# Kernel tuning notes

Measured on AMD Instinct MI355X. Metric: run time of the kernel, lower is better.

Reference implementation:

```python
import jax, jax.numpy as jnp
import numpy as np

CS = 128            # config.chunk_size
K = 8               # config.k + 1
EPS = 1e-6          # config.eps
L = K * CS          # extended_len = 1024


def setup_inputs() -> dict:
    key = jax.random.key(0)
    k1, k2 = jax.random.split(key)
    B, T, E = 2, 8192, 256
    x = jax.random.normal(k1, (B, T, E), dtype=jnp.float32)
    # xavier_normal_ on [CS, L]: std = sqrt(2 / (fan_in + fan_out))
    std = np.sqrt(2.0 / (CS + L)).astype(np.float32)
    down_proj = jax.random.normal(k2, (CS, L), dtype=jnp.float32) * std
    return {"x": x, "down_proj": down_proj}


def reference(x, down_proj):
    B, T, E = x.shape
    N = T // CS  # T chosen divisible by CS, so the pad branch is a no-op
    chunks = x.reshape(B, N, CS, E)

    # --- per-chunk retrieval scores (vectorized over the causal chunk loop) ---
    cn = chunks / (jnp.linalg.norm(chunks, axis=-1, keepdims=True) + EPS)
    # row-wise cosine sims between every pair of chunks: [B,N,N,CS,CS]
    sims = jnp.einsum('bice,bjde->bijcd', cn, cn)
    scores = sims.max(axis=-1).sum(axis=-1)              # [B,N,N]
    i_idx = jnp.arange(N)
    causal = i_idx[None, :] < i_idx[:, None]             # j < i allowed
    NEG = jnp.asarray(-1e9, x.dtype)
    scores = jnp.where(causal[None], scores, NEG)

    # --- topk selection, weights (num_sel_i = min(i, K-1)) ---
    vals, idx = jax.lax.top_k(scores, K - 1)             # descending, [B,N,K-1]
    num_sel = jnp.minimum(i_idx, K - 1)                  # [N]
    vmin_slot = jnp.clip(num_sel - 1, 0, K - 2)          # last valid slot = min of topk vals
    v_min = jnp.take_along_axis(vals, jnp.broadcast_to(vmin_slot[None, :, None], (B, N, 1)), axis=-1)
    slot = jnp.arange(K - 1)
    valid = slot[None, :] < num_sel[:, None]             # [N,K-1]
    w = jnp.where(valid[None], vals / (v_min + EPS), 0.0)  # [B,N,K-1]

    # --- weighted gather of selected chunks ---
    b_idx = jnp.arange(B)[:, None, None]
    sel = chunks[b_idx, idx]                             # [B,N,K-1,CS,E]
    weighted = sel * w[..., None, None]

    # --- left-pad to L: zeros occupy leftmost slots, then topk-ordered chunks, then cur ---
    shift = jnp.maximum(0, (K - 1) - i_idx)              # [N]
    src = jnp.clip(slot[None, :] - shift[:, None], 0, K - 2)   # [N,K-1]
    n_idx = jnp.arange(N)[None, :, None]
    arranged = weighted[b_idx, n_idx, src[None]]         # [B,N,K-1,CS,E]
    keep = slot[None, :] >= shift[:, None]
    arranged = jnp.where(keep[None, :, :, None, None], arranged, 0.0)

    ext = jnp.concatenate([arranged.reshape(B, N, (K - 1) * CS, E), chunks], axis=2)  # [B,N,L,E]
    # down_proj @ ext + x_chunks, then contract back to [B,T,E]
    out = jnp.einsum('cl,bnle->bnce', down_proj, ext) + chunks
    return out.reshape(B, N * CS, E)
```

## Files before the change

kernel.cpp:

```cpp
#include <hip/hip_runtime.h>
#include <hip/hip_bf16.h>

#define CS     128
#define EDIM   256
#define NBATCH 2
#define TLEN   8192
#define NCHUNK 64
#define LEXT   1024
#define KSEL   7

typedef __attribute__((ext_vector_type(8))) short   short8;
typedef __attribute__((ext_vector_type(4))) float   floatx4;

__device__ inline short bf16_of(float f) {
    __hip_bfloat16 h = __float2bfloat16(f);
    return *(short*)&h;
}
__device__ inline float f_of_bf16(short s) {
    __hip_bfloat16 h = *(__hip_bfloat16*)&s;
    return __bfloat162float(h);
}

__device__ inline void gl_lds16(const void* g, void* l) {
    __builtin_amdgcn_global_load_lds(
        (const __attribute__((address_space(1))) unsigned int*)g,
        (__attribute__((address_space(3))) unsigned int*)l, 16, 0, 0);
}

__global__ __launch_bounds__(256) void prep_kernel(const float* __restrict__ x,
                                                   const float* __restrict__ dp,
                                                   short* __restrict__ cn_hi,
                                                   short* __restrict__ cn_lo,
                                                   short* __restrict__ xt_hi,
                                                   short* __restrict__ dp_hi) {
    const int bx = blockIdx.x;
    if (bx >= 256) {
        int t = (bx - 256) * 256 + threadIdx.x;
#pragma unroll
        for (int u = 0; u < 16; ++u) {
            int idx = (t * 16 + u) * 4;
            float4 v = *(const float4*)(dp + idx);
            *(short4*)(dp_hi + idx) =
                make_short4(bf16_of(v.x), bf16_of(v.y), bf16_of(v.z), bf16_of(v.w));
        }
        return;
    }

    __shared__ float tile[64 * 257];
    const int b = bx >> 7, t0 = (bx & 127) * 64;
    const int tid = threadIdx.x;
    const int r = tid >> 2, q = tid & 3;

    const float* src = x + ((size_t)(b * TLEN + t0 + r)) * EDIM + q * 64;
    float* trow = &tile[r * 257 + q * 64];
    float s = 0.f;
#pragma unroll
    for (int u = 0; u < 16; ++u) {
        float4 v = *(const float4*)(src + u * 4);
        s += v.x * v.x + v.y * v.y + v.z * v.z + v.w * v.w;
        trow[u * 4 + 0] = v.x; trow[u * 4 + 1] = v.y;
        trow[u * 4 + 2] = v.z; trow[u * 4 + 3] = v.w;
    }
    s += __shfl_xor(s, 1);
    s += __shfl_xor(s, 2);
    const float rn = 1.0f / (sqrtf(s) + 1e-6f);

    short* ch = cn_hi + ((size_t)(b * TLEN + t0 + r)) * EDIM + q * 64;
    short* cl = cn_lo + ((size_t)(b * TLEN + t0 + r)) * EDIM + q * 64;
#pragma unroll
    for (int u = 0; u < 16; ++u) {
        short hs[4], ls[4];
#pragma unroll
        for (int k2 = 0; k2 < 4; ++k2) {
            float c = trow[u * 4 + k2] * rn;
            hs[k2] = bf16_of(c);
            ls[k2] = bf16_of(c - f_of_bf16(hs[k2]));
        }
        *(short4*)(ch + u * 4) = make_short4(hs[0], hs[1], hs[2], hs[3]);
        *(short4*)(cl + u * 4) = make_short4(ls[0], ls[1], ls[2], ls[3]);
    }
    __syncthreads();

    const int g16 = tid >> 4, tq = tid & 15;
#pragma unroll
    for (int it = 0; it < 16; ++it) {
        int e = g16 + it * 16;
        short hs2[4];
#pragma unroll
        for (int g = 0; g < 4; ++g)
            hs2[g] = bf16_of(tile[(tq * 4 + g) * 257 + e]);
        *(short4*)(xt_hi + ((size_t)(b * EDIM + e)) * TLEN + t0 + tq * 4)
            = make_short4(hs2[0], hs2[1], hs2[2], hs2[3]);
    }
}

__global__ __launch_bounds__(256) void scores_mfma(const short* __restrict__ cn_hi,
                                                   const short* __restrict__ cn_lo,
                                                   float* __restrict__ scores) {
    __shared__ short tiles[4][4096];
    double* red2  = (double*)&tiles[0][0];
    float*  redbuf = (float*)&tiles[0][8];

    const int p = blockIdx.x, b = blockIdx.y;
    int i = (int)((1.0f + sqrtf(1.0f + 8.0f * (float)p)) * 0.5f);
    while (i * (i - 1) / 2 > p) --i;
    while (i * (i + 1) / 2 <= p) ++i;
    const int j = p - i * (i - 1) / 2;

    const int tid  = threadIdx.x;
    const int w    = tid >> 6, lane = tid & 63;
    const int wr   = w >> 1, wc = w & 1;
    const int quad = lane >> 4, l15 = lane & 15;

    const short* sarr  = (w & 1) ? cn_lo : cn_hi;
    const size_t sbase = ((size_t)b * TLEN + ((w >> 1) ? j : i) * CS) * EDIM;
    const int rr  = lane >> 2;
    const int c16 = (lane & 3) * 8;
    const int csw = c16 ^ (((rr >> 1) & 3) * 8);
    const int q8  = (quad ^ ((l15 >> 1) & 3)) * 8;

    floatx4 acc[4][4];
#pragma unroll
    for (int rt = 0; rt < 4; ++rt)
#pragma unroll
        for (int ct = 0; ct < 4; ++ct) acc[rt][ct] = (floatx4){0.f, 0.f, 0.f, 0.f};

    for (int ks = 0; ks < 8; ++ks) {
        const short* gsrc = sarr + sbase + ks * 32 + csw;
        short* ldst = &tiles[w][0];
#pragma unroll
        for (int t = 0; t < 8; ++t)
            gl_lds16(gsrc + (size_t)(16 * t + rr) * EDIM, ldst + t * 512);
        __syncthreads();

        short8 bh[4], bl[4];
#pragma unroll
        for (int ct = 0; ct < 4; ++ct) {
            int r = wc * 64 + ct * 16 + l15;
            bh[ct] = *(const short8*)&tiles[2][r * 32 + q8];
            bl[ct] = *(const short8*)&tiles[3][r * 32 + q8];
        }
#pragma unroll
        for (int rt = 0; rt < 4; ++rt) {
            int r = wr * 64 + rt * 16 + l15;
            short8 ah = *(const short8*)&tiles[0][r * 32 + q8];
            short8 al = *(const short8*)&tiles[1][r * 32 + q8];
#pragma unroll
            for (int ct = 0; ct < 4; ++ct) {
                acc[rt][ct] = __builtin_amdgcn_mfma_f32_16x16x32_bf16(ah, bh[ct], acc[rt][ct], 0, 0, 0);
                acc[rt][ct] = __builtin_amdgcn_mfma_f32_16x16x32_bf16(ah, bl[ct], acc[rt][ct], 0, 0, 0);
                acc[rt][ct] = __builtin_amdgcn_mfma_f32_16x16x32_bf16(al, bh[ct], acc[rt][ct], 0, 0, 0);
            }
        }
        __syncthreads();
    }

#pragma unroll
    for (int rt = 0; rt < 4; ++rt) {
        float m[4];
#pragma unroll
        for (int reg = 0; reg < 4; ++reg) {
            float mm = acc[rt][0][reg];
#pragma unroll
            for (int ct = 1; ct < 4; ++ct) mm = fmaxf(mm, acc[rt][ct][reg]);
            m[reg] = mm;
        }
#pragma unroll
        for (int off = 1; off < 16; off <<= 1)
#pragma unroll
            for (int reg = 0; reg < 4; ++reg) m[reg] = fmaxf(m[reg], __shfl_xor(m[reg], off));
        if (l15 == 0) {
#pragma unroll
            for (int reg = 0; reg < 4; ++reg)
                redbuf[wc * 128 + wr * 64 + rt * 16 + quad * 4 + reg] = m[reg];
        }
    }
    __syncthreads();

    double part = 0.0;
    if (tid < 128) part = (double)fmaxf(redbuf[tid], redbuf[128 + tid]);
#pragma unroll
    for (int off = 1; off < 64; off <<= 1) part += __shfl_xor(part, off);
    if (lane == 0 && w < 2) red2[w] = part;
    __syncthreads();
    if (tid == 0) scores[(b * NCHUNK + i) * NCHUNK + j] = (float)(red2[0] + red2[1]);
}

__global__ __launch_bounds__(256) void out_mfma(const float* __restrict__ x,
                                                const short* __restrict__ dph,
                                                const short* __restrict__ xth,
                                                const float* __restrict__ scores,
                                                float* __restrict__ out) {
    __shared__ short As[2][128 * 32];
    __shared__ short Bs[2][64 * 32];
    __shared__ int   slist[8], sslot[8], snum;
    __shared__ float swei[8];

    const int eq = blockIdx.x, n = blockIdx.y, b = blockIdx.z;
    const int e0 = eq * 64;
    const int tid  = threadIdx.x;
    const int w    = tid >> 6, lane = tid & 63;
    const int wr   = w >> 1, wc = w & 1;
    const int quad = lane >> 4, l15 = lane & 15;
    const int rr   = lane >> 2;
    const int c16  = (lane & 3) * 8;
    const int csw  = c16 ^ (((rr >> 1) & 3) * 8);
    const int q8   = (quad ^ ((l15 >> 1) & 3)) * 8;

    if (w == 0) {
        const float* srow = scores + (b * NCHUNK + n) * NCHUNK;
        const int nsel = n < KSEL ? n : KSEL;
        float v = (lane < n) ? srow[lane] : -3.0e38f;
        float vals[KSEL];
        int   idxs[KSEL];
        for (int s2 = 0; s2 < nsel; ++s2) {
            float bv = v; int bi = lane;
#pragma unroll
            for (int off = 1; off < 64; off <<= 1) {
                float ov = __shfl_xor(bv, off);
                int   oi = __shfl_xor(bi, off);
                if (ov > bv || (ov == bv && oi < bi)) { bv = ov; bi = oi; }
            }
            vals[s2] = bv; idxs[s2] = bi;
            if (lane == bi) v = -3.0e38f;
        }
        if (lane == 0) {
            float vmin = (nsel > 0) ? vals[nsel - 1] : 0.0f;
            float inv  = 1.0f / (vmin + 1e-6f);
            int shift  = KSEL - nsel;
            int c = 0;
            for (int s2 = 0; s2 < 8; ++s2) {
                int jj; float ww;
                if (s2 < KSEL) {
                    int tt = s2 - shift;
                    if (tt >= 0) { jj = idxs[tt]; ww = vals[tt] * inv; }
                    else         { jj = -1;       ww = 0.0f; }
                } else { jj = n; ww = 1.0f; }
                if (jj >= 0) { slist[c] = jj; sslot[c] = s2; swei[c] = ww; ++c; }
            }
            snum = c;
        }
    }
    __syncthreads();
    const int NS = snum * 4;

    auto stage = [&](int st, int bf) {
        int sv = st >> 2, kk = st & 3;
        if (w < 2) {
            const short* gsrc = dph + (size_t)(sslot[sv] * 128 + kk * 32) + csw;
#pragma unroll
            for (int t = 0; t < 4; ++t)
                gl_lds16(gsrc + (size_t)(w * 64 + t * 16 + rr) * LEXT,
                         &As[bf][(w * 64 + t * 16) * 32]);
        } else {
            const short* gsrc = xth + ((size_t)(b * EDIM + e0)) * TLEN
                                + (size_t)(slist[sv] * CS + kk * 32) + csw;
#pragma unroll
            for (int t = 0; t < 2; ++t)
                gl_lds16(gsrc + (size_t)((w - 2) * 32 + t * 16 + rr) * TLEN,
                         &Bs[bf][((w - 2) * 32 + t * 16) * 32]);
        }
    };

    floatx4 accT[4][2], accP[4][2];
#pragma unroll
    for (int rt = 0; rt < 4; ++rt)
#pragma unroll
        for (int ct = 0; ct < 2; ++ct) accT[rt][ct] = (floatx4){0.f, 0.f, 0.f, 0.f};

    stage(0, 0);
    __syncthreads();

    int buf = 0;
    for (int st = 0; st < NS; ++st) {
        if (st + 1 < NS) stage(st + 1, buf ^ 1);

        if ((st & 3) == 0) {
#pragma unroll
            for (int rt = 0; rt < 4; ++rt)
#pragma unroll
                for (int ct = 0; ct < 2; ++ct) accP[rt][ct] = (floatx4){0.f, 0.f, 0.f, 0.f};
        }

        short8 bh[2];
#pragma unroll
        for (int ct = 0; ct < 2; ++ct) {
            int e = wc * 32 + ct * 16 + l15;
            bh[ct] = *(const short8*)&Bs[buf][e * 32 + q8];
        }
#pragma unroll
        for (int rt = 0; rt < 4; ++rt) {
            int r = wr * 64 + rt * 16 + l15;
            short8 ah = *(const short8*)&As[buf][r * 32 + q8];
#pragma unroll
            for (int ct = 0; ct < 2; ++ct)
                accP[rt][ct] = __builtin_amdgcn_mfma_f32_16x16x32_bf16(ah, bh[ct], accP[rt][ct], 0, 0, 0);
        }

        if ((st & 3) == 3) {
            float wcur = swei[st >> 2];
#pragma unroll
            for (int rt = 0; rt < 4; ++rt)
#pragma unroll
                for (int ct = 0; ct < 2; ++ct)
#pragma unroll
                    for (int reg = 0; reg < 4; ++reg)
                        accT[rt][ct][reg] += wcur * accP[rt][ct][reg];
        }
        __syncthreads();
        buf ^= 1;
    }

#pragma unroll
    for (int rt = 0; rt < 4; ++rt)
#pragma unroll
        for (int ct = 0; ct < 2; ++ct) {
#pragma unroll
            for (int reg = 0; reg < 4; ++reg) {
                int row = wr * 64 + rt * 16 + quad * 4 + reg;
                int col = wc * 32 + ct * 16 + l15;
                size_t o = ((size_t)(b * TLEN + n * CS + row)) * EDIM + e0 + col;
                out[o] = accT[rt][ct][reg] + x[o];
            }
        }
}

extern "C" void kernel_launch(void* const* d_in, const int* in_sizes, int n_in,
                              void* d_out, int out_size, void* d_ws, size_t ws_size,
                              hipStream_t stream) {
    const float* x  = (const float*)d_in[0];
    const float* dp = (const float*)d_in[1];
    float* out = (float*)d_out;

    char* ws = (char*)d_ws;
    short* cn_hi  = (short*)(ws);
    short* cn_lo  = (short*)(ws + (8u << 20));
    short* xt_hi  = (short*)(ws + (16u << 20));
    short* dp_hi  = (short*)(ws + (24u << 20));
    float* scores = (float*)(ws + (25u << 20));

    prep_kernel <<<dim3(264), 256, 0, stream>>>(x, dp, cn_hi, cn_lo, xt_hi, dp_hi);
    scores_mfma <<<dim3(NCHUNK * (NCHUNK - 1) / 2, NBATCH), 256, 0, stream>>>(cn_hi, cn_lo, scores);
    out_mfma    <<<dim3(4, NCHUNK, NBATCH), 256, 0, stream>>>(x, dp_hi, xt_hi, scores, out);
}
```

Before: 214.0 us.

## Fuse three kernels into one persistent cooperative kernel with grid syncs

Merges the prep, scores and output phases into a single cooperative persistent kernel that loops over work units with grid-stride loops and separates the phases with grid-wide barriers. The goal is to drop the launch gaps and tail effects between the three kernels. The prep phase is also restructured: row normalisation now uses one wave per row with shuffle reductions, and the transpose uses smaller 64x64 tiles. The cost is grid-sync overhead, occupancy capped by the 32KB shared buffer, and fewer blocks than the original scores launch. It falls back to the old three-launch path if the cooperative launch fails.

```diff
diff --git a/kernel.cpp b/kernel.cpp
--- a/kernel.cpp
+++ b/kernel.cpp
@@ -1,5 +1,8 @@
 #include <hip/hip_runtime.h>
 #include <hip/hip_bf16.h>
+#include <hip/hip_cooperative_groups.h>
+
+namespace cg = cooperative_groups;
 
 #define CS     128
 #define EDIM   256
@@ -25,6 +28,300 @@
     __builtin_amdgcn_global_load_lds(
         (const __attribute__((address_space(1))) unsigned int*)g,
         (__attribute__((address_space(3))) unsigned int*)l, 16, 0, 0);
+}
+
+__global__ __launch_bounds__(256) void mega_kernel(const float* __restrict__ x,
+                                                   const float* __restrict__ dp,
+                                                   short* __restrict__ cn_hi,
+                                                   short* __restrict__ cn_lo,
+                                                   short* __restrict__ xt_hi,
+                                                   short* __restrict__ dp_hi,
+                                                   float* __restrict__ scores,
+                                                   float* __restrict__ out) {
+    __shared__ __align__(16) char smem[32768];
+    cg::grid_group gg = cg::this_grid();
+
+    const int tid  = threadIdx.x;
+    const int bid  = blockIdx.x;
+    const int gdim = gridDim.x;
+    const int w    = tid >> 6, lane = tid & 63;
+    const int quad = lane >> 4, l15 = lane & 15;
+    const int rr   = lane >> 2, c16 = (lane & 3) * 8;
+    const int csw  = c16 ^ (((rr >> 1) & 3) * 8);
+    const int q8   = (quad ^ ((l15 >> 1) & 3)) * 8;
+
+    for (int u = bid; u < 2056; u += gdim) {
+        if (u < 1024) {
+#pragma unroll
+            for (int pass = 0; pass < 4; ++pass) {
+                int row = u * 16 + w * 4 + pass;
+                const float4 v = ((const float4*)(x + (size_t)row * EDIM))[lane];
+                float s = v.x * v.x + v.y * v.y + v.z * v.z + v.w * v.w;
+#pragma unroll
+                for (int off = 1; off < 64; off <<= 1) s += __shfl_xor(s, off);
+                float rn = 1.0f / (sqrtf(s) + 1e-6f);
+                float c[4] = {v.x * rn, v.y * rn, v.z * rn, v.w * rn};
+                short hs[4], ls[4];
+#pragma unroll
+                for (int q = 0; q < 4; ++q) {
+                    hs[q] = bf16_of(c[q]);
+                    ls[q] = bf16_of(c[q] - f_of_bf16(hs[q]));
+                }
+                size_t o = (size_t)row * EDIM + lane * 4;
+                *(short4*)(cn_hi + o) = make_short4(hs[0], hs[1], hs[2], hs[3]);
+                *(short4*)(cn_lo + o) = make_short4(ls[0], ls[1], ls[2], ls[3]);
+            }
+        } else if (u < 1032) {
+            int t = (u - 1024) * 256 + tid;
+#pragma unroll
+            for (int k = 0; k < 16; ++k) {
+                int idx = (t * 16 + k) * 4;
+                float4 v = *(const float4*)(dp + idx);
+                *(short4*)(dp_hi + idx) =
+                    make_short4(bf16_of(v.x), bf16_of(v.y), bf16_of(v.z), bf16_of(v.w));
+            }
+        } else {
+            float* tile = (float*)smem;
+            int ut = u - 1032;
+            int b2 = ut >> 9, et = (ut >> 7) & 3, tt2 = ut & 127;
+            int e0 = et * 64, t0 = tt2 * 64;
+            int r2 = tid >> 2, c4 = (tid & 3) * 16;
+            const float* src = x + ((size_t)(b2 * TLEN + t0 + r2)) * EDIM + e0 + c4;
+#pragma unroll
+            for (int k = 0; k < 4; ++k)
+                *(float4*)&tile[r2 * 68 + c4 + k * 4] = *(const float4*)(src + k * 4);
+            __syncthreads();
+            int e = tid >> 2, tq = tid & 3;
+            short hs2[16];
+#pragma unroll
+            for (int g = 0; g < 16; ++g) hs2[g] = bf16_of(tile[(tq * 16 + g) * 68 + e]);
+            short* xd = xt_hi + ((size_t)(b2 * EDIM + e0 + e)) * TLEN + t0 + tq * 16;
+#pragma unroll
+            for (int q4 = 0; q4 < 4; ++q4)
+                *(short4*)(xd + q4 * 4) =
+                    make_short4(hs2[q4*4], hs2[q4*4+1], hs2[q4*4+2], hs2[q4*4+3]);
+            __syncthreads();
+        }
+    }
+    gg.sync();
+
+    {
+        short (*tiles)[4096] = (short(*)[4096])smem;
+        double* red2  = (double*)smem;
+        float*  redbuf = (float*)(smem + 16);
+
+        for (int u = bid; u < 4032; u += gdim) {
+            const int b = u & 1, p = u >> 1;
+            int i = (int)((1.0f + sqrtf(1.0f + 8.0f * (float)p)) * 0.5f);
+            while (i * (i - 1) / 2 > p) --i;
+            while (i * (i + 1) / 2 <= p) ++i;
+            const int j = p - i * (i - 1) / 2;
+
+            const short* sarr  = (w & 1) ? cn_lo : cn_hi;
+            const size_t sbase = ((size_t)b * TLEN + ((w >> 1) ? j : i) * CS) * EDIM;
+            const int wr = w >> 1, wc = w & 1;
+
+            floatx4 acc[4][4];
+#pragma unroll
+            for (int rt = 0; rt < 4; ++rt)
+#pragma unroll
+                for (int ct = 0; ct < 4; ++ct) acc[rt][ct] = (floatx4){0.f, 0.f, 0.f, 0.f};
+
+            for (int ks = 0; ks < 8; ++ks) {
+                const short* gsrc = sarr + sbase + ks * 32 + csw;
+                short* ldst = &tiles[w][0];
+#pragma unroll
+                for (int t = 0; t < 8; ++t)
+                    gl_lds16(gsrc + (size_t)(16 * t + rr) * EDIM, ldst + t * 512);
+                __syncthreads();
+
+                short8 bh[4], bl[4];
+#pragma unroll
+                for (int ct = 0; ct < 4; ++ct) {
+                    int r = wc * 64 + ct * 16 + l15;
+                    bh[ct] = *(const short8*)&tiles[2][r * 32 + q8];
+                    bl[ct] = *(const short8*)&tiles[3][r * 32 + q8];
+                }
+#pragma unroll
+                for (int rt = 0; rt < 4; ++rt) {
+                    int r = wr * 64 + rt * 16 + l15;
+                    short8 ah = *(const short8*)&tiles[0][r * 32 + q8];
+                    short8 al = *(const short8*)&tiles[1][r * 32 + q8];
+#pragma unroll
+                    for (int ct = 0; ct < 4; ++ct) {
+                        acc[rt][ct] = __builtin_amdgcn_mfma_f32_16x16x32_bf16(ah, bh[ct], acc[rt][ct], 0, 0, 0);
+                        acc[rt][ct] = __builtin_amdgcn_mfma_f32_16x16x32_bf16(ah, bl[ct], acc[rt][ct], 0, 0, 0);
+                        acc[rt][ct] = __builtin_amdgcn_mfma_f32_16x16x32_bf16(al, bh[ct], acc[rt][ct], 0, 0, 0);
+                    }
+                }
+                __syncthreads();
+            }
+
+#pragma unroll
+            for (int rt = 0; rt < 4; ++rt) {
+                float m[4];
+#pragma unroll
+                for (int reg = 0; reg < 4; ++reg) {
+                    float mm = acc[rt][0][reg];
+#pragma unroll
+                    for (int ct = 1; ct < 4; ++ct) mm = fmaxf(mm, acc[rt][ct][reg]);
+                    m[reg] = mm;
+                }
+#pragma unroll
+                for (int off = 1; off < 16; off <<= 1)
+#pragma unroll
+                    for (int reg = 0; reg < 4; ++reg) m[reg] = fmaxf(m[reg], __shfl_xor(m[reg], off));
+                if (l15 == 0) {
+#pragma unroll
+                    for (int reg = 0; reg < 4; ++reg)
+                        redbuf[wc * 128 + wr * 64 + rt * 16 + quad * 4 + reg] = m[reg];
+                }
+            }
+            __syncthreads();
+
+            double part = 0.0;
+            if (tid < 128) part = (double)fmaxf(redbuf[tid], redbuf[128 + tid]);
+#pragma unroll
+            for (int off = 1; off < 64; off <<= 1) part += __shfl_xor(part, off);
+            if (lane == 0 && w < 2) red2[w] = part;
+            __syncthreads();
+            if (tid == 0) scores[(b * NCHUNK + i) * NCHUNK + j] = (float)(red2[0] + red2[1]);
+        }
+    }
+    gg.sync();
+
+    {
+        short* As    = (short*)smem;
+        short* Bs    = (short*)(smem + 16384);
+        int*   slist = (int*)(smem + 24576);
+        int*   sslot = (int*)(smem + 24608);
+        float* swei  = (float*)(smem + 24640);
+        int*   snum  = (int*)(smem + 24672);
+
+        for (int u = bid; u < 512; u += gdim) {
+            const int eq = u & 3, n = (u >> 2) & 63, b = u >> 8;
+            const int e0 = eq * 64;
+            const int wr = w >> 1, wc = w & 1;
+
+            if (w == 0) {
+                const float* srow = scores + (b * NCHUNK + n) * NCHUNK;
+                const int nsel = n < KSEL ? n : KSEL;
+                float v = (lane < n) ? srow[lane] : -3.0e38f;
+                float vals[KSEL];
+                int   idxs[KSEL];
+                for (int s2 = 0; s2 < nsel; ++s2) {
+                    float bv = v; int bi = lane;
+#pragma unroll
+                    for (int off = 1; off < 64; off <<= 1) {
+                        float ov = __shfl_xor(bv, off);
+                        int   oi = __shfl_xor(bi, off);
+                        if (ov > bv || (ov == bv && oi < bi)) { bv = ov; bi = oi; }
+                    }
+                    vals[s2] = bv; idxs[s2] = bi;
+                    if (lane == bi) v = -3.0e38f;
+                }
+                if (lane == 0) {
+                    float vmin = (nsel > 0) ? vals[nsel - 1] : 0.0f;
+                    float inv  = 1.0f / (vmin + 1e-6f);
+                    int shift  = KSEL - nsel;
+                    int c = 0;
+                    for (int s2 = 0; s2 < 8; ++s2) {
+                        int jj; float ww;
+                        if (s2 < KSEL) {
+                            int tt = s2 - shift;
+                            if (tt >= 0) { jj = idxs[tt]; ww = vals[tt] * inv; }
+                            else         { jj = -1;       ww = 0.0f; }
+                        } else { jj = n; ww = 1.0f; }
+                        if (jj >= 0) { slist[c] = jj; sslot[c] = s2; swei[c] = ww; ++c; }
+                    }
+                    *snum = c;
+                }
+            }
+            __syncthreads();
+            const int NS = (*snum) * 4;
+
+            auto stage = [&](int st, int bf) {
+                int sv = st >> 2, kk = st & 3;
+                if (w < 2) {
+                    const short* gsrc = dp_hi + (size_t)(sslot[sv] * 128 + kk * 32) + csw;
+#pragma unroll
+                    for (int t = 0; t < 4; ++t)
+                        gl_lds16(gsrc + (size_t)(w * 64 + t * 16 + rr) * LEXT,
+                                 As + bf * 4096 + (w * 64 + t * 16) * 32);
+                } else {
+                    const short* gsrc = xt_hi + ((size_t)(b * EDIM + e0)) * TLEN
+                                        + (size_t)(slist[sv] * CS + kk * 32) + csw;
+#pragma unroll
+                    for (int t = 0; t < 2; ++t)
+                        gl_lds16(gsrc + (size_t)((w - 2) * 32 + t * 16 + rr) * TLEN,
+                                 Bs + bf * 2048 + ((w - 2) * 32 + t * 16) * 32);
+                }
+            };
+
+            floatx4 accT[4][2], accP[4][2];
+#pragma unroll
+            for (int rt = 0; rt < 4; ++rt)
+#pragma unroll
+                for (int ct = 0; ct < 2; ++ct) accT[rt][ct] = (floatx4){0.f, 0.f, 0.f, 0.f};
+
+            stage(0, 0);
+            __syncthreads();
+
+            int buf = 0;
+            for (int st = 0; st < NS; ++st) {
+                if (st + 1 < NS) stage(st + 1, buf ^ 1);
+
+                if ((st & 3) == 0) {
+#pragma unroll
+                    for (int rt = 0; rt < 4; ++rt)
+#pragma unroll
+                        for (int ct = 0; ct < 2; ++ct) accP[rt][ct] = (floatx4){0.f, 0.f, 0.f, 0.f};
+                }
+
+                short8 bh[2];
+#pragma unroll
+                for (int ct = 0; ct < 2; ++ct) {
+                    int e = wc * 32 + ct * 16 + l15;
+                    bh[ct] = *(const short8*)&Bs[buf * 2048 + e * 32 + q8];
+                }
+#pragma unroll
+                for (int rt = 0; rt < 4; ++rt) {
+                    int r = wr * 64 + rt * 16 + l15;
+                    short8 ah = *(const short8*)&As[buf * 4096 + r * 32 + q8];
+#pragma unroll
+                    for (int ct = 0; ct < 2; ++ct)
+                        accP[rt][ct] = __builtin_amdgcn_mfma_f32_16x16x32_bf16(ah, bh[ct], accP[rt][ct], 0, 0, 0);
+                }
+
+                if ((st & 3) == 3) {
+                    float wcur = swei[st >> 2];
+#pragma unroll
+                    for (int rt = 0; rt < 4; ++rt)
+#pragma unroll
+                        for (int ct = 0; ct < 2; ++ct)
+#pragma unroll
+                            for (int reg = 0; reg < 4; ++reg)
+                                accT[rt][ct][reg] += wcur * accP[rt][ct][reg];
+                }
+                __syncthreads();
+                buf ^= 1;
+            }
+
+#pragma unroll
+            for (int rt = 0; rt < 4; ++rt)
+#pragma unroll
+                for (int ct = 0; ct < 2; ++ct) {
+#pragma unroll
+                    for (int reg = 0; reg < 4; ++reg) {
+                        int row = wr * 64 + rt * 16 + quad * 4 + reg;
+                        int col = wc * 32 + ct * 16 + l15;
+                        size_t o = ((size_t)(b * TLEN + n * CS + row)) * EDIM + e0 + col;
+                        out[o] = accT[rt][ct][reg] + x[o];
+                    }
+                }
+            __syncthreads();
+        }
+    }
 }
 
 __global__ __launch_bounds__(256) void prep_kernel(const float* __restrict__ x,
@@ -45,12 +342,10 @@
         }
         return;
     }
-
     __shared__ float tile[64 * 257];
     const int b = bx >> 7, t0 = (bx & 127) * 64;
     const int tid = threadIdx.x;
     const int r = tid >> 2, q = tid & 3;
-
     const float* src = x + ((size_t)(b * TLEN + t0 + r)) * EDIM + q * 64;
     float* trow = &tile[r * 257 + q * 64];
     float s = 0.f;
@@ -64,7 +359,6 @@
     s += __shfl_xor(s, 1);
     s += __shfl_xor(s, 2);
     const float rn = 1.0f / (sqrtf(s) + 1e-6f);
-
     short* ch = cn_hi + ((size_t)(b * TLEN + t0 + r)) * EDIM + q * 64;
     short* cl = cn_lo + ((size_t)(b * TLEN + t0 + r)) * EDIM + q * 64;
 #pragma unroll
@@ -80,7 +374,6 @@
         *(short4*)(cl + u * 4) = make_short4(ls[0], ls[1], ls[2], ls[3]);
     }
     __syncthreads();
-
     const int g16 = tid >> 4, tq = tid & 15;
 #pragma unroll
     for (int it = 0; it < 16; ++it) {
@@ -111,7 +404,6 @@
     const int w    = tid >> 6, lane = tid & 63;
     const int wr   = w >> 1, wc = w & 1;
     const int quad = lane >> 4, l15 = lane & 15;
-
     const short* sarr  = (w & 1) ? cn_lo : cn_hi;
     const size_t sbase = ((size_t)b * TLEN + ((w >> 1) ? j : i) * CS) * EDIM;
     const int rr  = lane >> 2;
@@ -132,7 +424,6 @@
         for (int t = 0; t < 8; ++t)
             gl_lds16(gsrc + (size_t)(16 * t + rr) * EDIM, ldst + t * 512);
         __syncthreads();
-
         short8 bh[4], bl[4];
 #pragma unroll
         for (int ct = 0; ct < 4; ++ct) {
@@ -154,7 +445,6 @@
         }
         __syncthreads();
     }
-
 #pragma unroll
     for (int rt = 0; rt < 4; ++rt) {
         float m[4];
@@ -176,7 +466,6 @@
         }
     }
     __syncthreads();
-
     double part = 0.0;
     if (tid < 128) part = (double)fmaxf(redbuf[tid], redbuf[128 + tid]);
 #pragma unroll
@@ -274,14 +563,12 @@
     int buf = 0;
     for (int st = 0; st < NS; ++st) {
         if (st + 1 < NS) stage(st + 1, buf ^ 1);
-
         if ((st & 3) == 0) {
 #pragma unroll
             for (int rt = 0; rt < 4; ++rt)
 #pragma unroll
                 for (int ct = 0; ct < 2; ++ct) accP[rt][ct] = (floatx4){0.f, 0.f, 0.f, 0.f};
         }
-
         short8 bh[2];
 #pragma unroll
         for (int ct = 0; ct < 2; ++ct) {
@@ -296,7 +583,6 @@
             for (int ct = 0; ct < 2; ++ct)
                 accP[rt][ct] = __builtin_amdgcn_mfma_f32_16x16x32_bf16(ah, bh[ct], accP[rt][ct], 0, 0, 0);
         }
-
         if ((st & 3) == 3) {
             float wcur = swei[st >> 2];
 #pragma unroll
@@ -310,7 +596,6 @@
         __syncthreads();
         buf ^= 1;
     }
-
 #pragma unroll
     for (int rt = 0; rt < 4; ++rt)
 #pragma unroll
@@ -339,6 +624,19 @@
     short* dp_hi  = (short*)(ws + (24u << 20));
     float* scores = (float*)(ws + (25u << 20));
 
+    int nb = 0;
+    hipError_t qe = hipOccupancyMaxActiveBlocksPerMultiprocessor(&nb, mega_kernel, 256, 0);
+    if (qe == hipSuccess && nb >= 1) {
+        int grid = nb * 256;
+        if (grid > 1024) grid = 1024;
+        void* args[] = {(void*)&x, (void*)&dp, (void*)&cn_hi, (void*)&cn_lo,
+                        (void*)&xt_hi, (void*)&dp_hi, (void*)&scores, (void*)&out};
+        hipError_t le = hipLaunchCooperativeKernel(mega_kernel, dim3(grid), dim3(256),
+                                                   args, 0u, stream);
+        if (le == hipSuccess) return;
+        (void)hipGetLastError();
+    }
+
     prep_kernel <<<dim3(264), 256, 0, stream>>>(x, dp, cn_hi, cn_lo, xt_hi, dp_hi);
     scores_mfma <<<dim3(NCHUNK * (NCHUNK - 1) / 2, NBATCH), 256, 0, stream>>>(cn_hi, cn_lo, scores);
     out_mfma    <<<dim3(4, NCHUNK, NBATCH), 256, 0, stream>>>(x, dp_hi, xt_hi, scores, out);
```

Result: no change. 214.0 us (-0.0%).
